# Optimization experiments

Hardware: AMD Instinct MI355X
Metric: run time of the kernel (lower is better)

## Reference

```python
import math
import jax, jax.numpy as jnp
import numpy as np

C1, D, NUM_HEADS, K_CH = 150, 32, 4, 10
GLOBAL_TOPK_RATIO = 0.08


def _pos2d(h, w, dim):
    d2 = dim // 2
    div = jnp.exp(jnp.arange(0, d2, 2, dtype=jnp.float32) * (-(math.log(10000.0) / d2)))
    def axis_pe(n):
        ang = jnp.arange(n, dtype=jnp.float32)[:, None] * div[None, :]
        pe = jnp.zeros((n, d2), dtype=jnp.float32)
        pe = pe.at[:, 0::2].set(jnp.sin(ang))
        pe = pe.at[:, 1::2].set(jnp.cos(ang))
        return pe
    pe_y = axis_pe(h)  # [h, d2]
    pe_x = axis_pe(w)  # [w, d2]
    return jnp.concatenate([
        jnp.broadcast_to(pe_y[:, None, :], (h, w, d2)),
        jnp.broadcast_to(pe_x[None, :, :], (h, w, d2)),
    ], axis=-1)  # [h, w, dim]


def setup_inputs() -> dict:
    key = jax.random.key(0)
    ks = jax.random.split(key, 7)
    B = 1024
    return {
        "x": jax.random.uniform(ks[0], (B, 1, 28, 28), dtype=jnp.float32),
        "conv1_w": jax.random.normal(ks[1], (C1, 1, 9, 9), dtype=jnp.float32) * 0.05,
        "channel_embed": jax.random.normal(ks[2], (C1, D), dtype=jnp.float32) * 0.02,
        "in_proj_w": jax.random.normal(ks[3], (3 * D, D), dtype=jnp.float32) * (1.0 / math.sqrt(D)),
        "in_proj_b": jnp.zeros((3 * D,), dtype=jnp.float32),
        "out_proj_w": jax.random.normal(ks[4], (D, D), dtype=jnp.float32) * (1.0 / math.sqrt(D)),
        "out_proj_b": jnp.zeros((D,), dtype=jnp.float32),
    }


def reference(x, conv1_w, channel_embed, in_proj_w, in_proj_b, out_proj_w, out_proj_b):
    # conv1 + relu: [B,1,28,28] -> [B,150,14,14]
    A = jax.nn.relu(jax.lax.conv_general_dilated(
        x, conv1_w, window_strides=(2, 2), padding=((4, 4), (4, 4)),
        dimension_numbers=("NCHW", "OIHW", "NCHW")))
    B, C, H, W = A.shape
    total = C * H * W
    k_global = max(1, int(math.ceil(GLOBAL_TOPK_RATIO * total)))
    A_flat = A.reshape(B, -1)
    # global kthvalue threshold: k_global-th largest per sample
    thresh = jax.lax.top_k(A_flat, k_global)[0][:, -1:]
    A_global = (A_flat * (A_flat >= thresh)).reshape(B, C, H, W)
    # per-location channel top-k + scatter
    v = jnp.transpose(A_global, (0, 2, 3, 1))  # [B,H,W,C]
    topv, topi = jax.lax.top_k(v, K_CH)        # [B,H,W,k]
    N = B * H * W
    logits = jnp.zeros((N, C), v.dtype).at[
        jnp.arange(N)[:, None], topi.reshape(N, K_CH)
    ].set(topv.reshape(N, K_CH)).reshape(v.shape)
    # normalize by per-sample global max (guard zero)
    flat_logits = logits.reshape(B, -1)
    gmax = jnp.max(flat_logits, axis=1, keepdims=True)
    normed = jnp.where(gmax == 0, 0.0, flat_logits / jnp.where(gmax == 0, 1.0, gmax))
    sparse_weights = normed.reshape(logits.shape)  # [B,H,W,C]
    # channel embedding + 2D sinusoidal PE
    loc_emb = jnp.einsum("bhwc,cd->bhwd", sparse_weights, channel_embed)
    loc_emb = loc_emb + _pos2d(H, W, D)[None]
    seq = loc_emb.reshape(B, H * W, D)
    # 1-layer MHA (self-attention, batch_first)
    qkv = seq @ in_proj_w.T + in_proj_b  # [B,S,3D]
    q, k, vv = jnp.split(qkv, 3, axis=-1)
    hd = D // NUM_HEADS
    def heads(t):
        return jnp.transpose(t.reshape(B, H * W, NUM_HEADS, hd), (0, 2, 1, 3))
    q, k, vv = heads(q), heads(k), heads(vv)
    attn = jax.nn.softmax(jnp.einsum("bnsd,bntd->bnst", q, k) / math.sqrt(hd), axis=-1)
    ctx = jnp.einsum("bnst,bntd->bnsd", attn, vv)
    ctx = jnp.transpose(ctx, (0, 2, 1, 3)).reshape(B, H * W, D)
    attn_out = ctx @ out_proj_w.T + out_proj_b  # [B, 196, 32]
    return attn_out
```

## Files before the change

### kernel.cpp

```cpp
#include <hip/hip_runtime.h>
#include <math.h>

#define NC1 150
#define HW 196
#define NB 1024
#define DD 32
#define NHD 4
#define HDIM 8
#define KG 2352
#define KCH 10
#define CAP 48
#define CVS 49
#define CES 36
#define KVS 20

typedef float v2f __attribute__((ext_vector_type(2)));

__device__ __forceinline__ float dot32v(const v2f* __restrict__ xr2,
                                        const float* __restrict__ wr, float bias) {
  const float4* w4 = (const float4*)wr;
  v2f s0 = {bias, 0.f};
  v2f s1 = {0.f, 0.f};
#pragma unroll
  for (int e = 0; e < 8; ++e) {
    float4 w = w4[e];
    v2f wlo = {w.x, w.y}, whi = {w.z, w.w};
    s0 = __builtin_elementwise_fma(xr2[2 * e], wlo, s0);
    s1 = __builtin_elementwise_fma(xr2[2 * e + 1], whi, s1);
  }
  v2f s = s0 + s1;
  return s.x + s.y;
}

#define UNI_F 17552
#define XT_OFF 0
#define WT_OFF 8232
#define CV_OFF 0
#define CC_OFF 9604
#define CNT_OFF 11956
#define CE_OFF 12152

__global__ void prep2_kernel(const float* __restrict__ cw, float* __restrict__ wtg,
                             float* __restrict__ pos) {
  int i = blockIdx.x * 256 + threadIdx.x;
  if (i < HW * DD) {
    int s = i >> 5, d = i & 31;
    int h = s / 14, w = s % 14;
    int p = (d < 16) ? h : w;
    int dd = (d < 16) ? d : d - 16;
    int j = dd >> 1;
    float dv = expf(-(logf(10000.0f) / 16.0f) * (float)(2 * j));
    float ang = (float)p * dv;
    pos[i] = (dd & 1) ? cosf(ang) : sinf(ang);
    return;
  }
  int j = i - HW * DD;
  if (j < 84 * 152) {
    int k = j / 152, c = j - k * 152;
    wtg[j] = (k < 81 && c < NC1) ? cw[c * 81 + k] : 0.f;
  }
}

__global__ __launch_bounds__(1024, 8) void fused_kernel(const float* __restrict__ x,
                                                        const float* __restrict__ wtg,
                                                        const float* __restrict__ CE,
                                                        const float* __restrict__ pos,
                                                        float* __restrict__ seqo) {
  __shared__ alignas(16) float uni[UNI_F];
  __shared__ alignas(16) float xs[784];
  __shared__ unsigned hist[2048];
  __shared__ unsigned wsum[4];
  __shared__ unsigned s_prefix, s_krem, s_max;

  int b = blockIdx.x, tid = threadIdx.x;
  int lane = tid & 63, wid = tid >> 6;

  if (tid < 196) ((float4*)xs)[tid] = ((const float4*)(x + (size_t)b * 784))[tid];
  if (tid == 0) { s_prefix = 0u; s_krem = KG; s_max = 0u; }
  __syncthreads();

  int cg = tid / 49;
  int g  = tid - cg * 49;
  bool act = (tid < 931);
  float acc[4][8];
#pragma unroll
  for (int i = 0; i < 4; ++i)
#pragma unroll
    for (int j = 0; j < 8; ++j) acc[i][j] = 0.f;

  float* XT = uni + XT_OFF;
  float* WT = uni + WT_OFF;

  for (int kb = 0; kb < 84; kb += 42) {
    for (int i = tid; i < 42 * 196; i += 1024) {
      int kk = i / 196, s = i - kk * 196;
      int k = kb + kk;
      float v = 0.f;
      if (k < 81) {
        int ki = k / 9, kj = k - ki * 9;
        int h = s / 14, w = s - h * 14;
        int r = 2 * h - 4 + ki, c = 2 * w - 4 + kj;
        if (r >= 0 && r < 28 && c >= 0 && c < 28) v = xs[r * 28 + c];
      }
      XT[i] = v;
    }
    for (int i = tid; i < (42 * 152) / 4; i += 1024)
      ((float4*)WT)[i] = ((const float4*)(wtg + kb * 152))[i];
    __syncthreads();
    if (act) {
      const float* xtp = XT + 4 * g;
      const float* wtp = WT + 8 * cg;
#pragma unroll 7
      for (int kk = 0; kk < 42; ++kk) {
        float4 xv = *(const float4*)(xtp + kk * 196);
        float4 w0 = *(const float4*)(wtp + kk * 152);
        float4 w1 = *(const float4*)(wtp + kk * 152 + 4);
        float xa[4] = {xv.x, xv.y, xv.z, xv.w};
        float wa[8] = {w0.x, w0.y, w0.z, w0.w, w1.x, w1.y, w1.z, w1.w};
#pragma unroll
        for (int i = 0; i < 4; ++i)
#pragma unroll
          for (int j = 0; j < 8; ++j) acc[i][j] += xa[i] * wa[j];
      }
    }
    __syncthreads();
  }

#pragma unroll
  for (int i = 0; i < 4; ++i)
#pragma unroll
    for (int j = 0; j < 8; ++j) acc[i][j] = fmaxf(acc[i][j], 0.f);

  for (int pass = 0; pass < 3; ++pass) {
    hist[tid] = 0u; hist[tid + 1024] = 0u;
    __syncthreads();
    int shift = (pass == 0) ? 21 : (pass == 1 ? 10 : 0);
    int bits = (pass == 2) ? 10 : 11;
    unsigned mask = (1u << bits) - 1u;
    unsigned pfx = s_prefix;
    unsigned krem = s_krem;
    int hishift = shift + bits;
    if (pass == 0) {
      unsigned mymax = 0u;
#pragma unroll
      for (int i = 0; i < 4; ++i)
#pragma unroll
        for (int j = 0; j < 8; ++j) {
          unsigned u = __float_as_uint(acc[i][j]);
          mymax = max(mymax, u);
          if (u) atomicAdd(&hist[u >> 21], 1u);
        }
#pragma unroll
      for (int st = 32; st >= 1; st >>= 1)
        mymax = max(mymax, (unsigned)__shfl_xor((int)mymax, st));
      if (lane == 0) atomicMax(&s_max, mymax);
    } else {
#pragma unroll
      for (int i = 0; i < 4; ++i)
#pragma unroll
        for (int j = 0; j < 8; ++j) {
          unsigned u = __float_as_uint(acc[i][j]);
          if (u && (u >> hishift) == pfx) atomicAdd(&hist[(u >> shift) & mask], 1u);
        }
    }
    __syncthreads();
    int segsz = (1 << bits) >> 8;
    unsigned segv = 0u, sufv = 0u;
    if (tid < 256) {
      for (int j = 0; j < segsz; ++j) segv += hist[tid * segsz + j];
      sufv = segv;
#pragma unroll
      for (int st = 1; st < 64; st <<= 1) {
        unsigned o = (unsigned)__shfl_down((int)sufv, st);
        if (lane + st < 64) sufv += o;
      }
      if (lane == 0) wsum[wid] = sufv;
    }
    __syncthreads();
    if (tid < 256) {
      unsigned tail = 0u;
      for (int ww = wid + 1; ww < 4; ++ww) tail += wsum[ww];
      sufv += tail;
      unsigned above = sufv - segv;
      if (above < krem && sufv >= krem) {
        unsigned cum = above;
        int dsel = tid * segsz;
        for (int d2 = segsz - 1; d2 >= 0; --d2) {
          int dd = tid * segsz + d2;
          if (cum + hist[dd] >= krem) { dsel = dd; break; }
          cum += hist[dd];
        }
        s_prefix = (pfx << bits) | (unsigned)dsel;
        s_krem = krem - cum;
      }
    }
    __syncthreads();
  }

  float* candV = uni + CV_OFF;
  unsigned char* candC = (unsigned char*)(uni + CC_OFF);
  unsigned* cnt = (unsigned*)(uni + CNT_OFF);
  if (tid < 196) cnt[tid] = 0u;
  __syncthreads();
  float T = __uint_as_float(s_prefix);
  if (act) {
#pragma unroll
    for (int i = 0; i < 4; ++i) {
      int loc = 4 * g + i;
#pragma unroll
      for (int j = 0; j < 8; ++j) {
        float v = acc[i][j];
        if (v >= T && v > 0.f) {
          unsigned slot = atomicAdd(&cnt[loc], 1u);
          if (slot < CAP) {
            candV[loc * CVS + slot] = v;
            candC[loc * CAP + slot] = (unsigned char)(8 * cg + j);
          }
        }
      }
    }
  }
  __syncthreads();

  float* CEs = uni + CE_OFF;
  if (tid >= 196) {
    for (int i = tid - 196; i < NC1 * 32; i += 1024 - 196) {
      int c = i >> 5, e = i & 31;
      CEs[c * CES + e] = CE[i];
    }
  }
  float tv[KCH]; int tc[KCH];
  if (tid < 196) {
    int loc = tid;
    unsigned n = cnt[loc]; if (n > CAP) n = CAP;
#pragma unroll
    for (int k = 0; k < KCH; ++k) { tv[k] = 0.f; tc[k] = 0; }
    for (unsigned jj = 0; jj < n; ++jj) {
      float v = candV[loc * CVS + jj];
      int c = candC[loc * CAP + jj];
      if (v > tv[KCH - 1] || (v == tv[KCH - 1] && c < tc[KCH - 1])) {
        float iv = v; int ic = c;
#pragma unroll
        for (int j = 0; j < KCH; ++j) {
          bool gt = (iv > tv[j]) || (iv == tv[j] && ic < tc[j]);
          float nv = gt ? iv : tv[j]; int nc = gt ? ic : tc[j];
          float ov = gt ? tv[j] : iv; int oc = gt ? tc[j] : ic;
          tv[j] = nv; tc[j] = nc; iv = ov; ic = oc;
        }
      }
    }
  }
  __syncthreads();

  if (tid < 196) {
    float gm = __uint_as_float(s_max);
    float gi = (gm == 0.0f) ? 0.0f : 1.0f / gm;
    float acc2[32];
#pragma unroll
    for (int e = 0; e < 32; ++e) acc2[e] = 0.f;
#pragma unroll
    for (int k = 0; k < KCH; ++k) {
      float v = tv[k];
      const float4* cr = (const float4*)(CEs + tc[k] * CES);
#pragma unroll
      for (int e4 = 0; e4 < 8; ++e4) {
        float4 cv = cr[e4];
        acc2[e4 * 4 + 0] += v * cv.x;
        acc2[e4 * 4 + 1] += v * cv.y;
        acc2[e4 * 4 + 2] += v * cv.z;
        acc2[e4 * 4 + 3] += v * cv.w;
      }
    }
    float* op = seqo + ((size_t)b * HW + tid) * DD;
    const float* pr = pos + tid * DD;
#pragma unroll
    for (int e4 = 0; e4 < 8; ++e4) {
      float4 pv = ((const float4*)pr)[e4];
      float4 o;
      o.x = acc2[e4 * 4 + 0] * gi + pv.x;
      o.y = acc2[e4 * 4 + 1] * gi + pv.y;
      o.z = acc2[e4 * 4 + 2] * gi + pv.z;
      o.w = acc2[e4 * 4 + 3] * gi + pv.w;
      ((float4*)op)[e4] = o;
    }
  }
}

__global__ __launch_bounds__(832, 3) void attn_kernel(const float* __restrict__ seq,
                                                      const float* __restrict__ Wqkv,
                                                      const float* __restrict__ bqkv,
                                                      float* __restrict__ ctxo) {
  __shared__ alignas(16) float kvs[NHD * HW * KVS];
  __shared__ alignas(16) float swq[96 * DD];
  __shared__ float sbq[96];
  __shared__ unsigned s_kk[NHD];

  int b = blockIdx.x, tid = threadIdx.x;
  int h = tid / HW;
  int s = tid - h * HW;
  bool act = (tid < NHD * HW);

  float xr[32];
  if (act) {
    const float* row = seq + ((size_t)b * HW + s) * DD;
#pragma unroll
    for (int e = 0; e < 8; ++e) {
      float4 f = ((const float4*)row)[e];
      xr[e * 4 + 0] = f.x; xr[e * 4 + 1] = f.y; xr[e * 4 + 2] = f.z; xr[e * 4 + 3] = f.w;
    }
  }
  for (int i = tid; i < (96 * DD) / 4; i += 832)
    ((float4*)swq)[i] = ((const float4*)Wqkv)[i];
  if (tid < 96) sbq[tid] = bqkv[tid];
  if (tid < NHD) s_kk[tid] = 0u;
  __syncthreads();

  float q[8]; float qq = 0.f;
  if (act) {
    float* kvrow = kvs + (h * HW + s) * KVS;
    {
      float ka[8]; float kk = 0.f;
#pragma unroll
      for (int d = 0; d < 8; ++d) {
        const float* wr = swq + (32 + h * HDIM + d) * DD;
        float acc = sbq[32 + h * HDIM + d];
#pragma unroll
        for (int e = 0; e < DD; e += 4) {
          float4 wv = *(const float4*)(wr + e);
          acc += xr[e + 0] * wv.x + xr[e + 1] * wv.y + xr[e + 2] * wv.z + xr[e + 3] * wv.w;
        }
        ka[d] = acc; kk += acc * acc;
      }
      float4 k0 = {ka[0], ka[1], ka[2], ka[3]}, k1 = {ka[4], ka[5], ka[6], ka[7]};
      ((float4*)kvrow)[0] = k0; ((float4*)kvrow)[1] = k1;
      atomicMax(&s_kk[h], __float_as_uint(kk));
    }
    {
      float va[8];
#pragma unroll
      for (int d = 0; d < 8; ++d) {
        const float* wr = swq + (64 + h * HDIM + d) * DD;
        float acc = sbq[64 + h * HDIM + d];
#pragma unroll
        for (int e = 0; e < DD; e += 4) {
          float4 wv = *(const float4*)(wr + e);
          acc += xr[e + 0] * wv.x + xr[e + 1] * wv.y + xr[e + 2] * wv.z + xr[e + 3] * wv.w;
        }
        va[d] = acc;
      }
      float4 v0 = {va[0], va[1], va[2], va[3]}, v1 = {va[4], va[5], va[6], va[7]};
      ((float4*)kvrow)[2] = v0; ((float4*)kvrow)[3] = v1;
    }
#pragma unroll
    for (int d = 0; d < 8; ++d) {
      const float* wr = swq + (h * HDIM + d) * DD;
      float acc = sbq[h * HDIM + d];
#pragma unroll
      for (int e = 0; e < DD; e += 4) {
        float4 wv = *(const float4*)(wr + e);
        acc += xr[e + 0] * wv.x + xr[e + 1] * wv.y + xr[e + 2] * wv.z + xr[e + 3] * wv.w;
      }
      q[d] = acc; qq += acc * acc;
    }
  }
  __syncthreads();
  if (!act) return;

  const float scaleL = 0.3535533905932738f * 1.4426950408889634f;
  float kkmax = __uint_as_float(s_kk[h]);
  float negML = -sqrtf(qq * kkmax) * scaleL;
  float l = 0.f;
  float c0 = 0.f, c1 = 0.f, c2 = 0.f, c3 = 0.f, c4 = 0.f, c5 = 0.f, c6 = 0.f, c7 = 0.f;
  const float4* kp = (const float4*)(kvs + (h * HW) * KVS);
  float4 k0 = kp[0], k1 = kp[1], v0 = kp[2], v1 = kp[3];
#pragma unroll 2
  for (int t = 0; t < HW - 1; ++t) {
    const float4* np = kp + 5;
    float4 nk0 = np[0], nk1 = np[1], nv0 = np[2], nv1 = np[3];
    float sc = q[0] * k0.x;
    sc = fmaf(q[1], k0.y, sc); sc = fmaf(q[2], k0.z, sc); sc = fmaf(q[3], k0.w, sc);
    sc = fmaf(q[4], k1.x, sc); sc = fmaf(q[5], k1.y, sc); sc = fmaf(q[6], k1.z, sc);
    sc = fmaf(q[7], k1.w, sc);
    float p = exp2f(fmaf(sc, scaleL, negML));
    l += p;
    c0 = fmaf(p, v0.x, c0); c1 = fmaf(p, v0.y, c1); c2 = fmaf(p, v0.z, c2);
    c3 = fmaf(p, v0.w, c3); c4 = fmaf(p, v1.x, c4); c5 = fmaf(p, v1.y, c5);
    c6 = fmaf(p, v1.z, c6); c7 = fmaf(p, v1.w, c7);
    k0 = nk0; k1 = nk1; v0 = nv0; v1 = nv1;
    kp = np;
  }
  {
    float sc = q[0] * k0.x;
    sc = fmaf(q[1], k0.y, sc); sc = fmaf(q[2], k0.z, sc); sc = fmaf(q[3], k0.w, sc);
    sc = fmaf(q[4], k1.x, sc); sc = fmaf(q[5], k1.y, sc); sc = fmaf(q[6], k1.z, sc);
    sc = fmaf(q[7], k1.w, sc);
    float p = exp2f(fmaf(sc, scaleL, negML));
    l += p;
    c0 = fmaf(p, v0.x, c0); c1 = fmaf(p, v0.y, c1); c2 = fmaf(p, v0.z, c2);
    c3 = fmaf(p, v0.w, c3); c4 = fmaf(p, v1.x, c4); c5 = fmaf(p, v1.y, c5);
    c6 = fmaf(p, v1.z, c6); c7 = fmaf(p, v1.w, c7);
  }
  float inv = 1.0f / l;
  float* op = ctxo + ((size_t)b * HW + s) * DD + h * HDIM;
  float4 o0, o1;
  o0.x = c0 * inv; o0.y = c1 * inv; o0.z = c2 * inv; o0.w = c3 * inv;
  o1.x = c4 * inv; o1.y = c5 * inv; o1.z = c6 * inv; o1.w = c7 * inv;
  ((float4*)op)[0] = o0; ((float4*)op)[1] = o1;
}

__global__ __launch_bounds__(256) void outproj_kernel(const float* __restrict__ ctx,
                                                      const float* __restrict__ Wo,
                                                      const float* __restrict__ bo,
                                                      float* __restrict__ out) {
  __shared__ float sw[32 * 32];
  __shared__ float sb2[32];
  int tid = threadIdx.x;
  for (int i = tid; i < 1024; i += 256) sw[i] = Wo[i];
  if (tid < 32) sb2[tid] = bo[tid];
  __syncthreads();
  size_t row = (size_t)blockIdx.x * 256 + tid;
  const float* cr = ctx + row * 32;
  v2f xr2[16];
#pragma unroll
  for (int e = 0; e < 8; ++e) {
    float4 f = ((const float4*)cr)[e];
    v2f lo = {f.x, f.y}, hi = {f.z, f.w};
    xr2[2 * e] = lo; xr2[2 * e + 1] = hi;
  }
  float* op = out + row * 32;
#pragma unroll
  for (int d4 = 0; d4 < 8; ++d4) {
    float4 o;
    float* oo = (float*)&o;
#pragma unroll
    for (int q = 0; q < 4; ++q) {
      int d = d4 * 4 + q;
      oo[q] = dot32v(xr2, sw + d * 32, sb2[d]);
    }
    ((float4*)op)[d4] = o;
  }
}

extern "C" void kernel_launch(void* const* d_in, const int* in_sizes, int n_in,
                              void* d_out, int out_size, void* d_ws, size_t ws_size,
                              hipStream_t stream) {
  const float* x  = (const float*)d_in[0];
  const float* cw = (const float*)d_in[1];
  const float* ce = (const float*)d_in[2];
  const float* wq = (const float*)d_in[3];
  const float* bq = (const float*)d_in[4];
  const float* wo = (const float*)d_in[5];
  const float* bo = (const float*)d_in[6];
  float* out = (float*)d_out;
  float* ws  = (float*)d_ws;

  float* ctx = ws;
  float* pos = ws + (size_t)NB * HW * DD;
  float* wtg = pos + HW * DD;

  prep2_kernel<<<(HW * DD + 84 * 152 + 255) / 256, 256, 0, stream>>>(cw, wtg, pos);
  fused_kernel<<<NB, 1024, 0, stream>>>(x, wtg, ce, pos, out);
  attn_kernel<<<NB, 832, 0, stream>>>(out, wq, bq, ctx);
  outproj_kernel<<<(NB * HW * DD) / (256 * 32), 256, 0, stream>>>(ctx, wo, bo, out);
}
```

Before: 401.2 us.

## Fuse conv/top-k/embedding kernel with attention kernel into one mega kernel

Merges the fused conv/topk/embedding kernel and the attention kernel into a single 1024-thread block per sample. A manually laid-out shared-memory buffer is reused across both phases, which removes one launch and a kernel boundary. The sequence is still written to global memory and re-read by the same block, so the round trip mostly stays in cache. It also simplifies the attention inner loop by dropping the manual prefetch, unrolling by 4 and using __expf. Risks include the larger shared-memory footprint under the 1024-thread bounds and losing the separate occupancy tuning the attention kernel had at 832 threads.

```diff
diff --git a/kernel.cpp b/kernel.cpp
--- a/kernel.cpp
+++ b/kernel.cpp
@@ -32,7 +32,13 @@
   return s.x + s.y;
 }
 
-#define UNI_F 17552
+#define SMEM_BYTES 75424
+#define XS_B   70208
+#define WSUM_B 73344
+#define SCTL_B 73360
+#define SWQ_B  62720
+#define SBQ_B  75008
+#define SKK_B  75392
 #define XT_OFF 0
 #define WT_OFF 8232
 #define CV_OFF 0
@@ -61,22 +67,26 @@
   }
 }
 
-__global__ __launch_bounds__(1024, 8) void fused_kernel(const float* __restrict__ x,
-                                                        const float* __restrict__ wtg,
-                                                        const float* __restrict__ CE,
-                                                        const float* __restrict__ pos,
-                                                        float* __restrict__ seqo) {
-  __shared__ alignas(16) float uni[UNI_F];
-  __shared__ alignas(16) float xs[784];
-  __shared__ unsigned hist[2048];
-  __shared__ unsigned wsum[4];
-  __shared__ unsigned s_prefix, s_krem, s_max;
+__global__ __launch_bounds__(1024, 8) void mega_kernel(const float* __restrict__ x,
+                                                       const float* __restrict__ wtg,
+                                                       const float* __restrict__ CE,
+                                                       const float* __restrict__ pos,
+                                                       const float* __restrict__ Wqkv,
+                                                       const float* __restrict__ bqkv,
+                                                       float* __restrict__ seqo,
+                                                       float* __restrict__ ctxo) {
+  __shared__ alignas(16) unsigned char smem[SMEM_BYTES];
+  float* uni = (float*)smem;
+  float* xs = (float*)(smem + XS_B);
+  unsigned* hist = (unsigned*)smem;
+  unsigned* wsum = (unsigned*)(smem + WSUM_B);
+  unsigned* sctl = (unsigned*)(smem + SCTL_B);
 
   int b = blockIdx.x, tid = threadIdx.x;
   int lane = tid & 63, wid = tid >> 6;
 
   if (tid < 196) ((float4*)xs)[tid] = ((const float4*)(x + (size_t)b * 784))[tid];
-  if (tid == 0) { s_prefix = 0u; s_krem = KG; s_max = 0u; }
+  if (tid == 0) { sctl[0] = 0u; sctl[1] = KG; sctl[2] = 0u; }
   __syncthreads();
 
   int cg = tid / 49;
@@ -137,8 +147,8 @@
     int shift = (pass == 0) ? 21 : (pass == 1 ? 10 : 0);
     int bits = (pass == 2) ? 10 : 11;
     unsigned mask = (1u << bits) - 1u;
-    unsigned pfx = s_prefix;
-    unsigned krem = s_krem;
+    unsigned pfx = sctl[0];
+    unsigned krem = sctl[1];
     int hishift = shift + bits;
     if (pass == 0) {
       unsigned mymax = 0u;
@@ -153,7 +163,7 @@
 #pragma unroll
       for (int st = 32; st >= 1; st >>= 1)
         mymax = max(mymax, (unsigned)__shfl_xor((int)mymax, st));
-      if (lane == 0) atomicMax(&s_max, mymax);
+      if (lane == 0) atomicMax(&sctl[2], mymax);
     } else {
 #pragma unroll
       for (int i = 0; i < 4; ++i)
@@ -190,8 +200,8 @@
           if (cum + hist[dd] >= krem) { dsel = dd; break; }
           cum += hist[dd];
         }
-        s_prefix = (pfx << bits) | (unsigned)dsel;
-        s_krem = krem - cum;
+        sctl[0] = (pfx << bits) | (unsigned)dsel;
+        sctl[1] = krem - cum;
       }
     }
     __syncthreads();
@@ -202,7 +212,7 @@
   unsigned* cnt = (unsigned*)(uni + CNT_OFF);
   if (tid < 196) cnt[tid] = 0u;
   __syncthreads();
-  float T = __uint_as_float(s_prefix);
+  float T = __uint_as_float(sctl[0]);
   if (act) {
 #pragma unroll
     for (int i = 0; i < 4; ++i) {
@@ -253,7 +263,7 @@
   __syncthreads();
 
   if (tid < 196) {
-    float gm = __uint_as_float(s_max);
+    float gm = __uint_as_float(sctl[2]);
     float gi = (gm == 0.0f) ? 0.0f : 1.0f / gm;
     float acc2[32];
 #pragma unroll
@@ -284,52 +294,47 @@
       ((float4*)op)[e4] = o;
     }
   }
-}
-
-__global__ __launch_bounds__(832, 3) void attn_kernel(const float* __restrict__ seq,
-                                                      const float* __restrict__ Wqkv,
-                                                      const float* __restrict__ bqkv,
-                                                      float* __restrict__ ctxo) {
-  __shared__ alignas(16) float kvs[NHD * HW * KVS];
-  __shared__ alignas(16) float swq[96 * DD];
-  __shared__ float sbq[96];
-  __shared__ unsigned s_kk[NHD];
-
-  int b = blockIdx.x, tid = threadIdx.x;
+  __syncthreads();
+
+  float* kvs = (float*)smem;
+  float* swq = (float*)(smem + SWQ_B);
+  float* sbq = (float*)(smem + SBQ_B);
+  unsigned* s_kk = (unsigned*)(smem + SKK_B);
+
   int h = tid / HW;
   int s = tid - h * HW;
-  bool act = (tid < NHD * HW);
+  bool aact = (tid < NHD * HW);
 
   float xr[32];
-  if (act) {
-    const float* row = seq + ((size_t)b * HW + s) * DD;
+  if (aact) {
+    const float* row = seqo + ((size_t)b * HW + s) * DD;
 #pragma unroll
     for (int e = 0; e < 8; ++e) {
       float4 f = ((const float4*)row)[e];
       xr[e * 4 + 0] = f.x; xr[e * 4 + 1] = f.y; xr[e * 4 + 2] = f.z; xr[e * 4 + 3] = f.w;
     }
   }
-  for (int i = tid; i < (96 * DD) / 4; i += 832)
+  for (int i = tid; i < (96 * DD) / 4; i += 1024)
     ((float4*)swq)[i] = ((const float4*)Wqkv)[i];
   if (tid < 96) sbq[tid] = bqkv[tid];
   if (tid < NHD) s_kk[tid] = 0u;
   __syncthreads();
 
   float q[8]; float qq = 0.f;
-  if (act) {
+  if (aact) {
     float* kvrow = kvs + (h * HW + s) * KVS;
     {
       float ka[8]; float kk = 0.f;
 #pragma unroll
       for (int d = 0; d < 8; ++d) {
         const float* wr = swq + (32 + h * HDIM + d) * DD;
-        float acc = sbq[32 + h * HDIM + d];
+        float a2 = sbq[32 + h * HDIM + d];
 #pragma unroll
         for (int e = 0; e < DD; e += 4) {
           float4 wv = *(const float4*)(wr + e);
-          acc += xr[e + 0] * wv.x + xr[e + 1] * wv.y + xr[e + 2] * wv.z + xr[e + 3] * wv.w;
-        }
-        ka[d] = acc; kk += acc * acc;
+          a2 += xr[e + 0] * wv.x + xr[e + 1] * wv.y + xr[e + 2] * wv.z + xr[e + 3] * wv.w;
+        }
+        ka[d] = a2; kk += a2 * a2;
       }
       float4 k0 = {ka[0], ka[1], ka[2], ka[3]}, k1 = {ka[4], ka[5], ka[6], ka[7]};
       ((float4*)kvrow)[0] = k0; ((float4*)kvrow)[1] = k1;
@@ -340,13 +345,13 @@
 #pragma unroll
       for (int d = 0; d < 8; ++d) {
         const float* wr = swq + (64 + h * HDIM + d) * DD;
-        float acc = sbq[64 + h * HDIM + d];
+        float a2 = sbq[64 + h * HDIM + d];
 #pragma unroll
         for (int e = 0; e < DD; e += 4) {
           float4 wv = *(const float4*)(wr + e);
-          acc += xr[e + 0] * wv.x + xr[e + 1] * wv.y + xr[e + 2] * wv.z + xr[e + 3] * wv.w;
-        }
-        va[d] = acc;
+          a2 += xr[e + 0] * wv.x + xr[e + 1] * wv.y + xr[e + 2] * wv.z + xr[e + 3] * wv.w;
+        }
+        va[d] = a2;
       }
       float4 v0 = {va[0], va[1], va[2], va[3]}, v1 = {va[4], va[5], va[6], va[7]};
       ((float4*)kvrow)[2] = v0; ((float4*)kvrow)[3] = v1;
@@ -354,47 +359,33 @@
 #pragma unroll
     for (int d = 0; d < 8; ++d) {
       const float* wr = swq + (h * HDIM + d) * DD;
-      float acc = sbq[h * HDIM + d];
+      float a2 = sbq[h * HDIM + d];
 #pragma unroll
       for (int e = 0; e < DD; e += 4) {
         float4 wv = *(const float4*)(wr + e);
-        acc += xr[e + 0] * wv.x + xr[e + 1] * wv.y + xr[e + 2] * wv.z + xr[e + 3] * wv.w;
-      }
-      q[d] = acc; qq += acc * acc;
-    }
-  }
-  __syncthreads();
-  if (!act) return;
-
-  const float scaleL = 0.3535533905932738f * 1.4426950408889634f;
+        a2 += xr[e + 0] * wv.x + xr[e + 1] * wv.y + xr[e + 2] * wv.z + xr[e + 3] * wv.w;
+      }
+      q[d] = a2; qq += a2 * a2;
+    }
+  }
+  __syncthreads();
+  if (!aact) return;
+
+  const float scale = 0.3535533905932738f;
   float kkmax = __uint_as_float(s_kk[h]);
-  float negML = -sqrtf(qq * kkmax) * scaleL;
+  float negM = -sqrtf(qq * kkmax) * scale;
   float l = 0.f;
   float c0 = 0.f, c1 = 0.f, c2 = 0.f, c3 = 0.f, c4 = 0.f, c5 = 0.f, c6 = 0.f, c7 = 0.f;
   const float4* kp = (const float4*)(kvs + (h * HW) * KVS);
-  float4 k0 = kp[0], k1 = kp[1], v0 = kp[2], v1 = kp[3];
-#pragma unroll 2
-  for (int t = 0; t < HW - 1; ++t) {
-    const float4* np = kp + 5;
-    float4 nk0 = np[0], nk1 = np[1], nv0 = np[2], nv1 = np[3];
+#pragma unroll 4
+  for (int t = 0; t < HW; ++t) {
+    float4 k0 = kp[0], k1 = kp[1], v0 = kp[2], v1 = kp[3];
+    kp += 5;
     float sc = q[0] * k0.x;
     sc = fmaf(q[1], k0.y, sc); sc = fmaf(q[2], k0.z, sc); sc = fmaf(q[3], k0.w, sc);
     sc = fmaf(q[4], k1.x, sc); sc = fmaf(q[5], k1.y, sc); sc = fmaf(q[6], k1.z, sc);
     sc = fmaf(q[7], k1.w, sc);
-    float p = exp2f(fmaf(sc, scaleL, negML));
-    l += p;
-    c0 = fmaf(p, v0.x, c0); c1 = fmaf(p, v0.y, c1); c2 = fmaf(p, v0.z, c2);
-    c3 = fmaf(p, v0.w, c3); c4 = fmaf(p, v1.x, c4); c5 = fmaf(p, v1.y, c5);
-    c6 = fmaf(p, v1.z, c6); c7 = fmaf(p, v1.w, c7);
-    k0 = nk0; k1 = nk1; v0 = nv0; v1 = nv1;
-    kp = np;
-  }
-  {
-    float sc = q[0] * k0.x;
-    sc = fmaf(q[1], k0.y, sc); sc = fmaf(q[2], k0.z, sc); sc = fmaf(q[3], k0.w, sc);
-    sc = fmaf(q[4], k1.x, sc); sc = fmaf(q[5], k1.y, sc); sc = fmaf(q[6], k1.z, sc);
-    sc = fmaf(q[7], k1.w, sc);
-    float p = exp2f(fmaf(sc, scaleL, negML));
+    float p = __expf(fmaf(sc, scale, negM));
     l += p;
     c0 = fmaf(p, v0.x, c0); c1 = fmaf(p, v0.y, c1); c2 = fmaf(p, v0.z, c2);
     c3 = fmaf(p, v0.w, c3); c4 = fmaf(p, v1.x, c4); c5 = fmaf(p, v1.y, c5);
@@ -459,7 +450,6 @@
   float* wtg = pos + HW * DD;
 
   prep2_kernel<<<(HW * DD + 84 * 152 + 255) / 256, 256, 0, stream>>>(cw, wtg, pos);
-  fused_kernel<<<NB, 1024, 0, stream>>>(x, wtg, ce, pos, out);
-  attn_kernel<<<NB, 832, 0, stream>>>(out, wq, bq, ctx);
+  mega_kernel<<<NB, 1024, 0, stream>>>(x, wtg, ce, pos, wq, bq, out, ctx);
   outproj_kernel<<<(NB * HW * DD) / (256 * 32), 256, 0, stream>>>(ctx, wo, bo, out);
 }
```

New measurement: 487.2 us. 21.4% more time.
